# Optimization experiments

Hardware: AMD Instinct MI355X
Metric: run time of the kernel (lower is better)

Reference implementation:

```python
import jax, jax.numpy as jnp
import numpy as np

B, S, D = 8, 2048, 128

def setup_inputs() -> dict:
    key = jax.random.key(0)
    kq, kk, kv = jax.random.split(key, 3)
    return {
        "query": jax.random.normal(kq, (B, S, D), dtype=jnp.float32),
        "key": jax.random.normal(kk, (B, S, D), dtype=jnp.float32),
        "value": jax.random.normal(kv, (B, S, D), dtype=jnp.float32),
    }

def reference(query, key, value):
    # softmax(QK^T / sqrt(d_k)) V, no mask, dropout=0
    d_k = query.shape[-1]
    scale = 1.0 / np.sqrt(d_k).astype(np.float32)
    # [B, Sq, Sk]
    attn_scores = jnp.einsum('bqd,bkd->bqk', query, key) * scale
    attn_weights = jax.nn.softmax(attn_scores, axis=-1)
    # [B, Sq, Dv]
    output = jnp.einsum('bqk,bkd->bqd', attn_weights, value)
    return (output, attn_weights)
```

## Files before the change

kernel.cpp:

```cpp
#include <hip/hip_runtime.h>
#include <hip/hip_bf16.h>

#define NB 8
#define SS 2048
#define DD 128
#define NQK (NB * SS * DD)

typedef __attribute__((ext_vector_type(8))) short bf16x8;
typedef __attribute__((ext_vector_type(16))) float f32x16;
typedef __attribute__((ext_vector_type(4))) float f32x4;
typedef __attribute__((ext_vector_type(4))) unsigned int uint4v;
typedef __attribute__((ext_vector_type(2))) unsigned int uint2v;

static constexpr float C1 = 0.08838834764831845f * 1.4426950408889634f;

#define MFMA32(a, b, c) __builtin_amdgcn_mfma_f32_32x32x16_bf16(a, b, c, 0, 0, 0)
#define PSWAP(a, b) __builtin_amdgcn_permlane32_swap(a, b, false, false)

#if __has_builtin(__builtin_amdgcn_exp2f)
#define EXP2 __builtin_amdgcn_exp2f
#else
#define EXP2 exp2f
#endif

__device__ __forceinline__ unsigned short f2bf(float x) {
  __hip_bfloat16 h = __float2bfloat16(x);
  unsigned short r;
  __builtin_memcpy(&r, &h, 2);
  return r;
}

__device__ __forceinline__ void nt_store4(const float* src, float* dst) {
  f32x4 v;
  __builtin_memcpy(&v, src, 16);
  __builtin_nontemporal_store(v, (f32x4*)dst);
}

__global__ __launch_bounds__(256)
void prep_kernel(const float* __restrict__ Q, const float* __restrict__ K,
                 const float* __restrict__ V, unsigned short* __restrict__ Qt,
                 unsigned short* __restrict__ Kt, unsigned short* __restrict__ Vt) {
  __shared__ __align__(16) float Tf[32][132];
  const int ti = blockIdx.x, b = blockIdx.y, role = blockIdx.z;
  const int tid = threadIdx.x;
  const float* src = role == 0 ? Q : (role == 1 ? K : V);
  {
    const int row = tid >> 3, seg = (tid & 7) * 16;
    const float4* sp = (const float4*)(src + ((size_t)b * SS + ti * 32 + row) * DD + seg);
#pragma unroll
    for (int j = 0; j < 4; ++j) *(float4*)&Tf[row][seg + 4 * j] = sp[j];
  }
  __syncthreads();
  if (role < 2) {
    unsigned short* dst = (role == 0 ? Qt : Kt) + ((size_t)b * 64 + ti) * 4096;
#pragma unroll
    for (int e = 0; e < 2; ++e) {
      const int c = 2 * tid + e, lq = c & 31, ck = c >> 5;
      const float4 a = *(const float4*)&Tf[lq][ck * 8];
      const float4 d = *(const float4*)&Tf[lq][ck * 8 + 4];
      bf16x8 o;
      o[0] = (short)f2bf(a.x); o[1] = (short)f2bf(a.y);
      o[2] = (short)f2bf(a.z); o[3] = (short)f2bf(a.w);
      o[4] = (short)f2bf(d.x); o[5] = (short)f2bf(d.y);
      o[6] = (short)f2bf(d.z); o[7] = (short)f2bf(d.w);
      *(bf16x8*)(dst + c * 8) = o;
    }
  } else {
    unsigned short* dst = Vt + ((size_t)b * 64 + ti) * 4096;
#pragma unroll
    for (int e = 0; e < 2; ++e) {
      const int chunk = 2 * tid + e, cc = chunk >> 7, d = chunk & 127;
      bf16x8 o;
#pragma unroll
      for (int j = 0; j < 8; ++j) o[j] = (short)f2bf(Tf[cc * 8 + j][d]);
      *(bf16x8*)(dst + chunk * 8) = o;
    }
  }
}

__global__ __launch_bounds__(256, 2)
void attn_kernel(const unsigned short* __restrict__ Qt,
                 const unsigned short* __restrict__ Kt,
                 const unsigned short* __restrict__ Vt,
                 float* __restrict__ W, float* __restrict__ Out) {
  __shared__ __align__(16) float PW[4][32][40];
  __shared__ __align__(16) float R[32][132];
  __shared__ float2 sms[4][32];

  const int bid = blockIdx.x;
  const int b = bid & 7, qb = bid >> 3;
  const int q0 = qb * 32;
  const int tid = threadIdx.x;
  const int lane = tid & 63, wv = tid >> 6;
  const int lq = lane & 31, h2 = lane >> 5;
  const int stag = (4 * qb + wv) & 15;
  const f32x16 ZERO16 = {0, 0, 0, 0, 0, 0, 0, 0, 0, 0, 0, 0, 0, 0, 0, 0};

  {
    float* Rf = &R[0][0];
    for (int idx = tid; idx < 32 * 132; idx += 256) Rf[idx] = 0.f;
  }

  const unsigned short* qbase = Qt + ((size_t)b * 64 + (q0 >> 5)) * 4096;
  bf16x8 qh[8];
#pragma unroll
  for (int ds = 0; ds < 8; ++ds)
    qh[ds] = *(const bf16x8*)(qbase + ((ds * 2 + h2) * 32 + lq) * 8);

  const unsigned short* const ktw = Kt + ((size_t)b * 64 + wv * 16) * 4096;
  const unsigned short* const vtw = Vt + ((size_t)b * 64 + wv * 16) * 4096;

  float m2 = -1e30f, s2 = 0.f;
#pragma unroll
  for (int kp = 0; kp < 8; ++kp) {
    const unsigned short* kb0 = ktw + (2 * kp) * 4096;
    const unsigned short* kb1 = kb0 + 4096;
    bf16x8 a0[8], a1[8];
#pragma unroll
    for (int ds = 0; ds < 8; ++ds) {
      a0[ds] = *(const bf16x8*)(kb0 + ((ds * 2 + h2) * 32 + lq) * 8);
      a1[ds] = *(const bf16x8*)(kb1 + ((ds * 2 + h2) * 32 + lq) * 8);
    }
    f32x16 acc0 = ZERO16, acc1 = ZERO16;
#pragma unroll
    for (int ds = 0; ds < 8; ++ds) {
      acc0 = MFMA32(a0[ds], qh[ds], acc0);
      acc1 = MFMA32(a1[ds], qh[ds], acc1);
    }
    float tm0 = acc0[0], tm1 = acc1[0];
#pragma unroll
    for (int r = 1; r < 16; ++r) {
      tm0 = fmaxf(tm0, acc0[r]);
      tm1 = fmaxf(tm1, acc1[r]);
    }
    const float nm2 = fmaxf(m2, fmaxf(tm0, tm1) * C1);
    float add = 0.f;
#pragma unroll
    for (int r = 0; r < 16; ++r)
      add += EXP2(fmaf(acc0[r], C1, -nm2)) + EXP2(fmaf(acc1[r], C1, -nm2));
    s2 = s2 * EXP2(m2 - nm2) + add;
    m2 = nm2;
  }
  {
    const float mo = __shfl_xor(m2, 32);
    const float so = __shfl_xor(s2, 32);
    const float nm = fmaxf(m2, mo);
    s2 = s2 * EXP2(m2 - nm) + so * EXP2(mo - nm);
    if (h2 == 0) sms[wv][lq] = make_float2(nm, s2);
  }
  __syncthreads();
  float lb;
  {
    float2 pj[4];
    float m = -1e30f;
#pragma unroll
    for (int j = 0; j < 4; ++j) {
      pj[j] = sms[j][lq];
      m = fmaxf(m, pj[j].x);
    }
    float s = 0.f;
#pragma unroll
    for (int j = 0; j < 4; ++j) s += pj[j].y * EXP2(pj[j].x - m);
    lb = -(m + __log2f(s));
  }

  float* pwwr[4];
#pragma unroll
  for (int g = 0; g < 4; ++g)
    pwwr[g] = &PW[wv][lq][(8 * g + 4 * h2 + lq * 4) & 31];
  const int gq8 = lane >> 3, gks = lane & 7;
  const float* pwrd[4];
  float* wgb[4];
#pragma unroll
  for (int i = 0; i < 4; ++i) {
    const int row = i * 8 + gq8;
    pwrd[i] = &PW[wv][row][(gks * 4 + row * 4) & 31];
    wgb[i] = W + ((size_t)b * SS + q0 + row) * SS + gks * 4;
  }

  f32x16 accO[4];
#pragma unroll
  for (int dt = 0; dt < 4; ++dt) accO[dt] = ZERO16;

  f32x16 acc = ZERO16;
  bf16x8 vb[8];
  {
    const unsigned short* k0 = ktw + stag * 4096;
    const unsigned short* v0 = vtw + stag * 4096;
    bf16x8 ah[8];
#pragma unroll
    for (int ds = 0; ds < 8; ++ds)
      ah[ds] = *(const bf16x8*)(k0 + ((ds * 2 + h2) * 32 + lq) * 8);
#pragma unroll
    for (int ds = 0; ds < 8; ++ds) acc = MFMA32(ah[ds], qh[ds], acc);
#pragma unroll
    for (int kk = 0; kk < 2; ++kk)
#pragma unroll
      for (int dt = 0; dt < 4; ++dt)
        vb[kk * 4 + dt] =
            *(const bf16x8*)(v0 + ((kk * 2 + h2) * 128 + dt * 32 + lq) * 8);
  }

  for (int kt = 0; kt < 16; ++kt) {
    const int lt = (kt + stag) & 15;
    const int kb = (wv * 16 + lt) * 32;
    bf16x8 ahn[8], vbn[8];
    if (kt < 15) {
      const int ln = (kt + 1 + stag) & 15;
      const unsigned short* kn = ktw + ln * 4096;
      const unsigned short* vn = vtw + ln * 4096;
#pragma unroll
      for (int ds = 0; ds < 8; ++ds)
        ahn[ds] = *(const bf16x8*)(kn + ((ds * 2 + h2) * 32 + lq) * 8);
#pragma unroll
      for (int kk = 0; kk < 2; ++kk)
#pragma unroll
        for (int dt = 0; dt < 4; ++dt)
          vbn[kk * 4 + dt] =
              *(const bf16x8*)(vn + ((kk * 2 + h2) * 128 + dt * 32 + lq) * 8);
    }
    unsigned int U[8];
#pragma unroll
    for (int g = 0; g < 4; ++g) {
      const float p0 = EXP2(fmaf(acc[4 * g + 0], C1, lb));
      const float p1 = EXP2(fmaf(acc[4 * g + 1], C1, lb));
      const float p2 = EXP2(fmaf(acc[4 * g + 2], C1, lb));
      const float p3 = EXP2(fmaf(acc[4 * g + 3], C1, lb));
      *(float4*)pwwr[g] = make_float4(p0, p1, p2, p3);
      U[2 * g] = (unsigned)f2bf(p0) | ((unsigned)f2bf(p1) << 16);
      U[2 * g + 1] = (unsigned)f2bf(p2) | ((unsigned)f2bf(p3) << 16);
    }
    f32x16 accn = ZERO16;
    if (kt < 15) {
#pragma unroll
      for (int ds = 0; ds < 8; ++ds) accn = MFMA32(ahn[ds], qh[ds], accn);
    }
#pragma unroll
    for (int i = 0; i < 4; ++i) nt_store4(pwrd[i], wgb[i] + kb);
    const uint2v s02 = PSWAP(U[0], U[2]);
    const uint2v s13 = PSWAP(U[1], U[3]);
    const uint2v s46 = PSWAP(U[4], U[6]);
    const uint2v s57 = PSWAP(U[5], U[7]);
    uint4v w0, w1;
    w0.x = s02.x; w0.y = s13.x; w0.z = s02.y; w0.w = s13.y;
    w1.x = s46.x; w1.y = s57.x; w1.z = s46.y; w1.w = s57.y;
    const bf16x8 pa0 = __builtin_bit_cast(bf16x8, w0);
    const bf16x8 pa1 = __builtin_bit_cast(bf16x8, w1);
#pragma unroll
    for (int dt = 0; dt < 4; ++dt) accO[dt] = MFMA32(pa0, vb[dt], accO[dt]);
#pragma unroll
    for (int dt = 0; dt < 4; ++dt) accO[dt] = MFMA32(pa1, vb[4 + dt], accO[dt]);
    acc = accn;
#pragma unroll
    for (int j = 0; j < 8; ++j) vb[j] = vbn[j];
  }

  __syncthreads();
#pragma unroll
  for (int ph = 0; ph < 4; ++ph) {
    if (wv == ph) {
#pragma unroll
      for (int dt = 0; dt < 4; ++dt) {
#pragma unroll
        for (int r = 0; r < 16; ++r) {
          const int q = (r & 3) + 8 * (r >> 2) + 4 * h2;
          R[q][dt * 32 + lq] += accO[dt][r];
        }
      }
    }
    __syncthreads();
  }
  {
    const int row = tid >> 3, c0 = (tid & 7) * 16;
    float* ob = Out + ((size_t)b * SS + q0 + row) * DD + c0;
#pragma unroll
    for (int j = 0; j < 4; ++j) nt_store4(&R[row][c0 + 4 * j], ob + 4 * j);
  }
}

extern "C" void kernel_launch(void* const* d_in, const int* in_sizes, int n_in,
                              void* d_out, int out_size, void* d_ws, size_t ws_size,
                              hipStream_t stream) {
  const float* Q = (const float*)d_in[0];
  const float* K = (const float*)d_in[1];
  const float* V = (const float*)d_in[2];
  float* out = (float*)d_out;
  float* W = out + (size_t)NQK;

  char* ws = (char*)d_ws;
  unsigned short* Qt = (unsigned short*)(ws);
  unsigned short* Kt = (unsigned short*)(ws + ((size_t)4 << 20));
  unsigned short* Vt = (unsigned short*)(ws + ((size_t)8 << 20));

  prep_kernel<<<dim3(64, 8, 3), 256, 0, stream>>>(Q, K, V, Qt, Kt, Vt);
  attn_kernel<<<512, 256, 0, stream>>>(Qt, Kt, Vt, W, out);
}
```

Before: 63.54 us.

## Batch attention-weight stores into 128-column rows and alias reduction buffer onto staging LDS

The staging buffer for softmax probabilities now holds four key tiles (128 columns) per wave. The global write of W happens once every four iterations, so each row store covers 512 contiguous bytes instead of 128. The output-reduction buffer R is aliased onto this staging buffer, and the first wave writes instead of accumulating, which removes the zero-init loop. The key-tile stagger is coarsened to multiples of four so that batched tiles stay contiguous. This increases LDS per block and makes stores burstier, which may affect occupancy and overlap with the MFMA work.

```diff
diff --git a/kernel.cpp b/kernel.cpp
--- a/kernel.cpp
+++ b/kernel.cpp
@@ -83,9 +83,9 @@
                  const unsigned short* __restrict__ Kt,
                  const unsigned short* __restrict__ Vt,
                  float* __restrict__ W, float* __restrict__ Out) {
-  __shared__ __align__(16) float PW[4][32][40];
-  __shared__ __align__(16) float R[32][132];
+  __shared__ __align__(16) float PW[4][32][132];
   __shared__ float2 sms[4][32];
+  float (*R)[132] = (float(*)[132]) & PW[0][0][0];
 
   const int bid = blockIdx.x;
   const int b = bid & 7, qb = bid >> 3;
@@ -93,13 +93,8 @@
   const int tid = threadIdx.x;
   const int lane = tid & 63, wv = tid >> 6;
   const int lq = lane & 31, h2 = lane >> 5;
-  const int stag = (4 * qb + wv) & 15;
+  const int stag4 = ((qb + wv) & 3) * 4;
   const f32x16 ZERO16 = {0, 0, 0, 0, 0, 0, 0, 0, 0, 0, 0, 0, 0, 0, 0, 0};
-
-  {
-    float* Rf = &R[0][0];
-    for (int idx = tid; idx < 32 * 132; idx += 256) Rf[idx] = 0.f;
-  }
 
   const unsigned short* qbase = Qt + ((size_t)b * 64 + (q0 >> 5)) * 4096;
   bf16x8 qh[8];
@@ -164,20 +159,6 @@
     lb = -(m + __log2f(s));
   }
 
-  float* pwwr[4];
-#pragma unroll
-  for (int g = 0; g < 4; ++g)
-    pwwr[g] = &PW[wv][lq][(8 * g + 4 * h2 + lq * 4) & 31];
-  const int gq8 = lane >> 3, gks = lane & 7;
-  const float* pwrd[4];
-  float* wgb[4];
-#pragma unroll
-  for (int i = 0; i < 4; ++i) {
-    const int row = i * 8 + gq8;
-    pwrd[i] = &PW[wv][row][(gks * 4 + row * 4) & 31];
-    wgb[i] = W + ((size_t)b * SS + q0 + row) * SS + gks * 4;
-  }
-
   f32x16 accO[4];
 #pragma unroll
   for (int dt = 0; dt < 4; ++dt) accO[dt] = ZERO16;
@@ -185,8 +166,8 @@
   f32x16 acc = ZERO16;
   bf16x8 vb[8];
   {
-    const unsigned short* k0 = ktw + stag * 4096;
-    const unsigned short* v0 = vtw + stag * 4096;
+    const unsigned short* k0 = ktw + stag4 * 4096;
+    const unsigned short* v0 = vtw + stag4 * 4096;
     bf16x8 ah[8];
 #pragma unroll
     for (int ds = 0; ds < 8; ++ds)
@@ -201,12 +182,15 @@
             *(const bf16x8*)(v0 + ((kk * 2 + h2) * 128 + dt * 32 + lq) * 8);
   }
 
+  const int fp = lq >> 3, fc = (lq & 7) * 4;
+  float* const wq0 = W + ((size_t)b * SS + q0) * SS + wv * 512;
+
   for (int kt = 0; kt < 16; ++kt) {
-    const int lt = (kt + stag) & 15;
-    const int kb = (wv * 16 + lt) * 32;
+    const int lt = (kt + stag4) & 15;
+    const int p = kt & 3;
     bf16x8 ahn[8], vbn[8];
     if (kt < 15) {
-      const int ln = (kt + 1 + stag) & 15;
+      const int ln = (kt + 1 + stag4) & 15;
       const unsigned short* kn = ktw + ln * 4096;
       const unsigned short* vn = vtw + ln * 4096;
 #pragma unroll
@@ -220,23 +204,36 @@
               *(const bf16x8*)(vn + ((kk * 2 + h2) * 128 + dt * 32 + lq) * 8);
     }
     unsigned int U[8];
-#pragma unroll
-    for (int g = 0; g < 4; ++g) {
-      const float p0 = EXP2(fmaf(acc[4 * g + 0], C1, lb));
-      const float p1 = EXP2(fmaf(acc[4 * g + 1], C1, lb));
-      const float p2 = EXP2(fmaf(acc[4 * g + 2], C1, lb));
-      const float p3 = EXP2(fmaf(acc[4 * g + 3], C1, lb));
-      *(float4*)pwwr[g] = make_float4(p0, p1, p2, p3);
-      U[2 * g] = (unsigned)f2bf(p0) | ((unsigned)f2bf(p1) << 16);
-      U[2 * g + 1] = (unsigned)f2bf(p2) | ((unsigned)f2bf(p3) << 16);
+    {
+      float* pwr = &PW[wv][lq][p * 32];
+#pragma unroll
+      for (int g = 0; g < 4; ++g) {
+        const float p0 = EXP2(fmaf(acc[4 * g + 0], C1, lb));
+        const float p1 = EXP2(fmaf(acc[4 * g + 1], C1, lb));
+        const float p2 = EXP2(fmaf(acc[4 * g + 2], C1, lb));
+        const float p3 = EXP2(fmaf(acc[4 * g + 3], C1, lb));
+        *(float4*)(pwr + ((8 * g + 4 * h2 + 4 * lq + 8 * p) & 31)) =
+            make_float4(p0, p1, p2, p3);
+        U[2 * g] = (unsigned)f2bf(p0) | ((unsigned)f2bf(p1) << 16);
+        U[2 * g + 1] = (unsigned)f2bf(p2) | ((unsigned)f2bf(p3) << 16);
+      }
     }
     f32x16 accn = ZERO16;
     if (kt < 15) {
 #pragma unroll
       for (int ds = 0; ds < 8; ++ds) accn = MFMA32(ahn[ds], qh[ds], accn);
     }
-#pragma unroll
-    for (int i = 0; i < 4; ++i) nt_store4(pwrd[i], wgb[i] + kb);
+    if (p == 3) {
+      asm volatile("" ::: "memory");
+      const int gb = ((kt & ~3) + stag4) & 15;
+      float* wcol = wq0 + (gb + fp) * 32 + fc;
+#pragma unroll
+      for (int ii = 0; ii < 16; ++ii) {
+        const int row = 2 * ii + h2;
+        nt_store4(&PW[wv][row][fp * 32 + ((fc + 4 * row + 8 * fp) & 31)],
+                  wcol + (size_t)row * SS);
+      }
+    }
     const uint2v s02 = PSWAP(U[0], U[2]);
     const uint2v s13 = PSWAP(U[1], U[3]);
     const uint2v s46 = PSWAP(U[4], U[6]);
@@ -264,7 +261,8 @@
 #pragma unroll
         for (int r = 0; r < 16; ++r) {
           const int q = (r & 3) + 8 * (r >> 2) + 4 * h2;
-          R[q][dt * 32 + lq] += accO[dt][r];
+          if (ph == 0) R[q][dt * 32 + lq] = accO[dt][r];
+          else         R[q][dt * 32 + lq] += accO[dt][r];
         }
       }
     }
```

After: 78.43 us. 23.4% more time.
